# Performance work log

Measured on AMD Instinct MI355X. Metric: run time of the kernel, lower is better.

## Reference

```python
import jax, jax.numpy as jnp
import numpy as np

SOFTMAX_TEMP = 0.01
WINDOW_SIZE = 2


def setup_inputs() -> dict:
    key = jax.random.key(0)
    k1, k2, k3, k4 = jax.random.split(key, 4)
    bsz, C, N, H, W = 8, 248, 512, 256, 256
    return {
        "keypoint_scores": jax.random.uniform(k1, (bsz, 1, N), dtype=jnp.float32),
        "keypoint_desc": jax.random.normal(k2, (bsz, C, N), dtype=jnp.float32),
        "scores_dense": jax.random.uniform(k3, (bsz, 1, H, W), dtype=jnp.float32),
        "desc_dense": jax.random.normal(k4, (bsz, C, H, W), dtype=jnp.float32),
    }


def reference(keypoint_scores, keypoint_desc, scores_dense, desc_dense):
    w = WINDOW_SIZE
    bsz, C, N = keypoint_desc.shape
    B = bsz // w  # batch_size (number of windows)
    H, Wd = desc_dense.shape[2], desc_dense.shape[3]
    HW = H * Wd

    # dense pixel coords: meshgrid 'ij' -> v over H, u over W; coords = stack(u, v)
    v_coord, u_coord = jnp.meshgrid(jnp.arange(H, dtype=jnp.float32),
                                    jnp.arange(Wd, dtype=jnp.float32), indexing="ij")
    coords = jnp.stack((u_coord.reshape(HW), v_coord.reshape(HW)), axis=1)  # [HW, 2]

    # source frame of each window: every window_size-th item, L2-normalized over C
    src = desc_dense[::w].reshape(B, C, HW)  # [B, C, HW]
    src = src / jnp.linalg.norm(src, axis=1, keepdims=True).clip(1e-12)

    # target frames: indices i*w + 1 .. i*w + w-1 for each window i
    tgt_ids = (jnp.arange(B)[:, None] * w + jnp.arange(1, w)[None, :]).reshape(-1)  # [B*(w-1)]
    tgt = keypoint_desc[tgt_ids].reshape(B, w - 1, C, N)  # [B, w-1, C, N]

    # similarity of each keypoint vs dense src grid; temperature softmax over grid
    match = jnp.einsum("bwcn,bch->bwnh", tgt, src)  # [B, w-1, N, HW]
    soft = jax.nn.softmax(match / SOFTMAX_TEMP, axis=-1)

    # expected 2D coordinate per keypoint
    pseudo = jnp.einsum("bwnh,hd->bwnd", soft, coords)  # [B, w-1, N, 2]
    pseudo_coords = pseudo.reshape(B * (w - 1), N, 2)

    return pseudo_coords, keypoint_scores[tgt_ids], tgt_ids
```

## Files before the change

kernel.cpp:

```cpp
#include <hip/hip_runtime.h>
#include <stdint.h>
#include <stddef.h>

#define C_DIM 248
#define N_KP 512
#define HW_PIX 65536
#define NWIN 4
#define NTILE 32
#define NQ 4
#define GROUPS32 2048
#define SCALE_LOG2 144.2695041f

typedef __attribute__((ext_vector_type(8))) _Float16 f16x8;
typedef __attribute__((ext_vector_type(4))) float f32x4;

__device__ __forceinline__ float fexp2(float x) {
    return __builtin_amdgcn_exp2f(x);
}

__global__ __launch_bounds__(256) void k_prep(const float* __restrict__ kd,
                                              f16x8* __restrict__ Bws) {
    int g = blockIdx.x * 256 + threadIdx.x;
    int c15 = g & 15;
    int l4 = (g >> 4) & 3;
    int kk = (g >> 6) & 7;
    int t  = (g >> 9) & 31;
    int b  = g >> 14;
    int col = t * 16 + c15;
    const float* base = kd + (size_t)(2 * b + 1) * C_DIM * N_KP;
    f16x8 hv;
    #pragma unroll
    for (int j = 0; j < 8; ++j) {
        int c = kk * 32 + l4 * 8 + j;
        float v = (c < C_DIM) ? base[(size_t)c * N_KP + col] : 0.0f;
        hv[j] = (_Float16)v;
    }
    Bws[(size_t)(b * 32 + t) * 512 + kk * 64 + l4 * 16 + c15] = hv;
}

__global__ __launch_bounds__(512, 1) void k_main(const float* __restrict__ dd,
                                                 const f16x8* __restrict__ Bws,
                                                 float4* __restrict__ partials) {
    int b = blockIdx.x >> 8;
    int grp = blockIdx.x & 255;
    int tid = threadIdx.x;
    int lane = tid & 63;
    int wave = tid >> 6;
    int l15 = lane & 15;
    int l4 = lane >> 4;
    int pw = grp * 256 + wave * 32;
    int g32 = grp * 8 + wave;

    __shared__ __align__(16) short Bbuf[2][32768];

    const f16x8* Bwin = Bws + (size_t)b * 32 * 512;
    #define STAGE(slot_, q_)                                                          \
        {                                                                             \
            const f16x8* src_ = Bwin + (size_t)(q_) * 4096;                           \
            _Pragma("unroll")                                                         \
            for (int i_ = 0; i_ < 8; ++i_) {                                          \
                __builtin_amdgcn_global_load_lds(                                     \
                    (const __attribute__((address_space(1))) void*)                   \
                        (src_ + i_ * 512 + wave * 64 + lane),                         \
                    (__attribute__((address_space(3))) void*)                         \
                        ((char*)&Bbuf[slot_][0] + (i_ * 512 + wave * 64) * 16),       \
                    16, 0, 0);                                                        \
            }                                                                         \
        }

    STAGE(0, 0)

    const float* srcp = dd + (size_t)(2 * b) * C_DIM * HW_PIX;
    f16x8 aH[2][8];
    float ss[2] = {0.f, 0.f};
    #pragma unroll
    for (int s = 0; s < 2; ++s) {
        #pragma unroll
        for (int kk = 0; kk < 8; ++kk) {
            #pragma unroll
            for (int j = 0; j < 8; ++j) {
                int c = kk * 32 + l4 * 8 + j;
                float v = (c < C_DIM) ? srcp[(size_t)c * HW_PIX + pw + s * 16 + l15] : 0.0f;
                ss[s] = fmaf(v, v, ss[s]);
                aH[s][kk][j] = (_Float16)v;
            }
        }
        ss[s] += __shfl_xor(ss[s], 16);
        ss[s] += __shfl_xor(ss[s], 32);
    }
    float srow[2][4];
    #pragma unroll
    for (int s = 0; s < 2; ++s) {
        #pragma unroll
        for (int r = 0; r < 4; ++r) {
            float ssr = __shfl(ss[s], l4 * 4 + r);
            srow[s][r] = SCALE_LOG2 / fmaxf(sqrtf(ssr), 1e-12f);
        }
    }
    float ubase = (float)((pw & 255) + l4 * 4);

    asm volatile("s_waitcnt vmcnt(0)" ::: "memory");
    __builtin_amdgcn_s_barrier();

    for (int q = 0; q < NQ; ++q) {
        if (q + 1 < NQ) STAGE((q + 1) & 1, q + 1)

        const short* qbase = &Bbuf[q & 1][0];
        #pragma unroll 2
        for (int tt = 0; tt < 8; ++tt) {
            int t = q * 8 + tt;
            const f16x8* Bt = (const f16x8*)(qbase + tt * 4096);
            f32x4 acc[2][2];
            #pragma unroll
            for (int s = 0; s < 2; ++s)
                #pragma unroll
                for (int qq = 0; qq < 2; ++qq) acc[s][qq] = (f32x4){0.f, 0.f, 0.f, 0.f};

            __builtin_amdgcn_s_setprio(1);
            #pragma unroll
            for (int kp = 0; kp < 4; ++kp) {
                f16x8 b0 = Bt[(2 * kp) * 64 + lane];
                f16x8 b1 = Bt[(2 * kp + 1) * 64 + lane];
                acc[0][0] = __builtin_amdgcn_mfma_f32_16x16x32_f16(aH[0][2 * kp], b0, acc[0][0], 0, 0, 0);
                acc[1][0] = __builtin_amdgcn_mfma_f32_16x16x32_f16(aH[1][2 * kp], b0, acc[1][0], 0, 0, 0);
                acc[0][1] = __builtin_amdgcn_mfma_f32_16x16x32_f16(aH[0][2 * kp + 1], b1, acc[0][1], 0, 0, 0);
                acc[1][1] = __builtin_amdgcn_mfma_f32_16x16x32_f16(aH[1][2 * kp + 1], b1, acc[1][1], 0, 0, 0);
            }
            __builtin_amdgcn_s_setprio(0);

            float lg[2][4];
            float m = -3.0e38f;
            #pragma unroll
            for (int s = 0; s < 2; ++s)
                #pragma unroll
                for (int r = 0; r < 4; ++r) {
                    lg[s][r] = (acc[s][0][r] + acc[s][1][r]) * srow[s][r];
                    m = fmaxf(m, lg[s][r]);
                }
            float d = 0.f, sx = 0.f;
            #pragma unroll
            for (int s = 0; s < 2; ++s)
                #pragma unroll
                for (int r = 0; r < 4; ++r) {
                    float e = fexp2(lg[s][r] - m);
                    d += e;
                    sx = fmaf(e, ubase + (float)(s * 16 + r), sx);
                }
            #pragma unroll
            for (int off = 16; off <= 32; off <<= 1) {
                float m2 = __shfl_xor(m, off);
                float d2 = __shfl_xor(d, off);
                float sx2 = __shfl_xor(sx, off);
                float Mn = fmaxf(m, m2);
                float c1 = fexp2(m - Mn);
                float c2 = fexp2(m2 - Mn);
                d  = d * c1 + d2 * c2;
                sx = sx * c1 + sx2 * c2;
                m = Mn;
            }
            if (lane < 16) {
                float4 p; p.x = m; p.y = d; p.z = sx; p.w = 0.f;
                partials[((size_t)b * GROUPS32 + g32) * 512 + t * 16 + l15] = p;
            }
        }

        if (q + 1 < NQ) {
            asm volatile("s_waitcnt vmcnt(8)" ::: "memory");
            __builtin_amdgcn_s_barrier();
        }
    }
    #undef STAGE
}

__global__ __launch_bounds__(256) void k_reduce(const float4* __restrict__ partials,
                                                const float* __restrict__ ksc,
                                                float* __restrict__ out) {
    int b = blockIdx.x >> 6;
    int kc = blockIdx.x & 63;
    int tid = threadIdx.x;
    int kpo = tid & 7;
    int gs = tid >> 3;
    int kp = kc * 8 + kpo;

    float M = -1e30f, D = 0.f, SX = 0.f, SY = 0.f;
    for (int g = gs; g < GROUPS32; g += 32) {
        float4 p = partials[((size_t)b * GROUPS32 + g) * 512 + kp];
        float vg = (float)(g >> 3);
        float Mn = fmaxf(M, p.x);
        float c1 = fexp2(M - Mn);
        float c2 = fexp2(p.x - Mn);
        D  = D  * c1 + p.y * c2;
        SX = SX * c1 + p.z * c2;
        SY = SY * c1 + vg * p.y * c2;
        M = Mn;
    }
    __shared__ float4 red[32][8];
    float4 me; me.x = M; me.y = D; me.z = SX; me.w = SY;
    red[gs][kpo] = me;
    __syncthreads();
    if (gs == 0) {
        #pragma unroll
        for (int w = 1; w < 32; ++w) {
            float4 p = red[w][kpo];
            float Mn = fmaxf(M, p.x);
            float c1 = fexp2(M - Mn);
            float c2 = fexp2(p.x - Mn);
            D  = D  * c1 + p.y * c2;
            SX = SX * c1 + p.z * c2;
            SY = SY * c1 + p.w * c2;
            M = Mn;
        }
        int flat = b * 512 + kp;
        out[flat * 2 + 0] = SX / D;
        out[flat * 2 + 1] = SY / D;
        out[4096 + flat] = ksc[(size_t)(2 * b + 1) * N_KP + kp];
    }
    if (blockIdx.x == 0 && tid < 4) out[6144 + tid] = (float)(2 * tid + 1);
}

extern "C" void kernel_launch(void* const* d_in, const int* in_sizes, int n_in,
                              void* d_out, int out_size, void* d_ws, size_t ws_size,
                              hipStream_t stream) {
    const float* kp_scores  = (const float*)d_in[0];
    const float* kp_desc    = (const float*)d_in[1];
    const float* desc_dense = (const float*)d_in[3];
    float* out = (float*)d_out;

    f16x8* Bws = (f16x8*)d_ws;
    float4* partials = (float4*)((char*)d_ws + (size_t)NWIN * 32 * 512 * 16);

    k_prep<<<256, 256, 0, stream>>>(kp_desc, Bws);
    k_main<<<NWIN * 256, 512, 0, stream>>>(desc_dense, Bws, partials);
    k_reduce<<<NWIN * 64, 256, 0, stream>>>(partials, kp_scores, out);
}
```

Before: 181.7 us.

## Pre-reduce per-wave softmax partials in LDS before writing to global

```diff
diff --git a/kernel.cpp b/kernel.cpp
--- a/kernel.cpp
+++ b/kernel.cpp
@@ -8,7 +8,7 @@
 #define NWIN 4
 #define NTILE 32
 #define NQ 4
-#define GROUPS32 2048
+#define GROUPS256 256
 #define SCALE_LOG2 144.2695041f
 
 typedef __attribute__((ext_vector_type(8))) _Float16 f16x8;
@@ -49,9 +49,9 @@
     int l15 = lane & 15;
     int l4 = lane >> 4;
     int pw = grp * 256 + wave * 32;
-    int g32 = grp * 8 + wave;
 
     __shared__ __align__(16) short Bbuf[2][32768];
+    __shared__ float4 Wst[8][128];
 
     const f16x8* Bwin = Bws + (size_t)b * 32 * 512;
     #define STAGE(slot_, q_)                                                          \
@@ -108,7 +108,6 @@
         const short* qbase = &Bbuf[q & 1][0];
         #pragma unroll 2
         for (int tt = 0; tt < 8; ++tt) {
-            int t = q * 8 + tt;
             const f16x8* Bt = (const f16x8*)(qbase + tt * 4096);
             f32x4 acc[2][2];
             #pragma unroll
@@ -160,14 +159,29 @@
             }
             if (lane < 16) {
                 float4 p; p.x = m; p.y = d; p.z = sx; p.w = 0.f;
-                partials[((size_t)b * GROUPS32 + g32) * 512 + t * 16 + l15] = p;
-            }
-        }
-
-        if (q + 1 < NQ) {
-            asm volatile("s_waitcnt vmcnt(8)" ::: "memory");
-            __builtin_amdgcn_s_barrier();
-        }
+                Wst[wave][tt * 16 + l15] = p;
+            }
+        }
+
+        asm volatile("s_waitcnt vmcnt(0) lgkmcnt(0)" ::: "memory");
+        __builtin_amdgcn_s_barrier();
+        if (tid < 128) {
+            float4 s0 = Wst[0][tid];
+            float M = s0.x, D = s0.y, SX = s0.z;
+            #pragma unroll
+            for (int w = 1; w < 8; ++w) {
+                float4 p = Wst[w][tid];
+                float Mn = fmaxf(M, p.x);
+                float c1 = fexp2(M - Mn);
+                float c2 = fexp2(p.x - Mn);
+                D  = D  * c1 + p.y * c2;
+                SX = SX * c1 + p.z * c2;
+                M = Mn;
+            }
+            float4 o; o.x = M; o.y = D; o.z = SX; o.w = 0.f;
+            partials[((size_t)b * GROUPS256 + grp) * 512 + q * 128 + tid] = o;
+        }
+        if (q + 1 < NQ) __builtin_amdgcn_s_barrier();
     }
     #undef STAGE
 }
@@ -183,9 +197,9 @@
     int kp = kc * 8 + kpo;
 
     float M = -1e30f, D = 0.f, SX = 0.f, SY = 0.f;
-    for (int g = gs; g < GROUPS32; g += 32) {
-        float4 p = partials[((size_t)b * GROUPS32 + g) * 512 + kp];
-        float vg = (float)(g >> 3);
+    for (int g = gs; g < GROUPS256; g += 32) {
+        float4 p = partials[((size_t)b * GROUPS256 + g) * 512 + kp];
+        float vg = (float)g;
         float Mn = fmaxf(M, p.x);
         float c1 = fexp2(M - Mn);
         float c2 = fexp2(p.x - Mn);
```

Result: faster. 161.4 us (median of 2 runs) (-11.2%).
